# Kernel optimization log

Measured on AMD Instinct MI355X. Metric: run time of the kernel, lower is better.

## Reference

```python
import jax, jax.numpy as jnp
import numpy as np

B, D_IN, D_EXP, D_TOW, N_EXP, N_TASK = 16384, 1024, 1024, 512, 8, 4


def setup_inputs() -> dict:
    key = jax.random.key(0)
    ks = jax.random.split(key, 8)
    s_in = 1.0 / np.sqrt(D_IN)
    s_exp = 1.0 / np.sqrt(D_EXP)
    s_tow = 1.0 / np.sqrt(D_TOW)
    return {
        "x": jax.random.normal(ks[0], (B, D_IN), jnp.float32),
        # gate: ParameterList of num_experts vectors of size input_size -> [D_IN, N_EXP] matrix
        "gate_w": jax.random.normal(ks[1], (D_IN, N_EXP), jnp.float32) * s_in,
        # per-expert SLP: Linear(input_size, expert_size) + ReLU
        "exp_w": jax.random.normal(ks[2], (N_EXP, D_IN, D_EXP), jnp.float32) * s_in,
        "exp_b": jax.random.normal(ks[3], (N_EXP, D_EXP), jnp.float32) * 0.01,
        # per-task tower MLP: Linear(expert_size, tower_size) + ReLU + Linear(tower_size, 1)
        "tw1": jax.random.normal(ks[4], (N_TASK, D_EXP, D_TOW), jnp.float32) * s_exp,
        "tb1": jax.random.normal(ks[5], (N_TASK, D_TOW), jnp.float32) * 0.01,
        "tw2": jax.random.normal(ks[6], (N_TASK, D_TOW, 1), jnp.float32) * s_tow,
        "tb2": jax.random.normal(ks[7], (N_TASK, 1), jnp.float32) * 0.01,
    }


def reference(x, gate_w, exp_w, exp_b, tw1, tb1, tw2, tb2):
    # gates = x @ gate (no softmax in original)        [B, E]
    gates = x @ gate_w
    # all experts in one batched GEMM                  [E, B, D_exp]
    h = jax.nn.relu(jnp.einsum("bi,eid->ebd", x, exp_w) + exp_b[:, None, :])
    # fused gate-weighted combine (replaces the nested Python loops)
    shared = jnp.einsum("be,ebd->bd", gates, h)        # [B, D_exp]
    # per-task towers, batched over tasks
    t = jax.nn.relu(jnp.einsum("bd,tdh->tbh", shared, tw1) + tb1[:, None, :])
    outs = jnp.einsum("tbh,tho->tbo", t, tw2) + tb2[:, None, :]  # [T, B, 1]
    return outs
```

## Files before the change

### kernel.cpp

```cpp
#include <hip/hip_runtime.h>
#include <hip/hip_bf16.h>

#define B_DIM   16384
#define D_IN    1024
#define D_EXP   1024
#define D_TOW   512
#define N_EXPT  8
#define N_TASK  4

typedef _Float16 f16x8 __attribute__((ext_vector_type(8)));
typedef _Float16 f16x4 __attribute__((ext_vector_type(4)));
typedef float    f32x4 __attribute__((ext_vector_type(4)));

__device__ __forceinline__ void gll16(const void* g, void* l) {
  __builtin_amdgcn_global_load_lds(
      (const __attribute__((address_space(1))) unsigned int*)g,
      (__attribute__((address_space(3))) unsigned int*)l,
      16, 0, 0);
}

__device__ __forceinline__ f16x8 ldfrag(const _Float16* sM, int rowbase, int ks, int lane) {
  int rl = rowbase + (lane & 15);
  int ch = ((ks << 2) + (lane >> 4)) ^ (rl & 7);
  return *(const f16x8*)&sM[rl * 64 + ch * 8];
}

__global__ __launch_bounds__(256) void prep_x_kernel(
    const float* __restrict__ x, const float* __restrict__ gw,
    _Float16* __restrict__ xh, float* __restrict__ gates)
{
  __shared__ float sred[4][8];
  const int t = threadIdx.x;
  const long row = blockIdx.x;
  float4 v = ((const float4*)(x + row * D_IN))[t];
  f16x4 h;
  h[0] = (_Float16)v.x; h[1] = (_Float16)v.y; h[2] = (_Float16)v.z; h[3] = (_Float16)v.w;
  ((f16x4*)(xh + row * D_IN))[t] = h;

  float g[8];
#pragma unroll
  for (int e = 0; e < 8; ++e) g[e] = 0.f;
  const float* wp = gw + (size_t)t * 4 * 8;
  float xs[4] = {v.x, v.y, v.z, v.w};
#pragma unroll
  for (int j = 0; j < 4; ++j)
#pragma unroll
    for (int e = 0; e < 8; ++e) g[e] += xs[j] * wp[j * 8 + e];

#pragma unroll
  for (int e = 0; e < 8; ++e) {
    g[e] += __shfl_xor(g[e], 1);  g[e] += __shfl_xor(g[e], 2);
    g[e] += __shfl_xor(g[e], 4);  g[e] += __shfl_xor(g[e], 8);
    g[e] += __shfl_xor(g[e], 16); g[e] += __shfl_xor(g[e], 32);
  }
  if ((t & 63) == 0) {
#pragma unroll
    for (int e = 0; e < 8; ++e) sred[t >> 6][e] = g[e];
  }
  __syncthreads();
  if (t < 8) gates[row * 8 + t] = sred[0][t] + sred[1][t] + sred[2][t] + sred[3][t];
}

__global__ __launch_bounds__(256) void transpose_cvt_kernel(
    const float* __restrict__ in, _Float16* __restrict__ outp, int K, int N)
{
  __shared__ float tile[64][65];
  const int t = threadIdx.x;
  const int tx = t & 63, ty = t >> 6;
  const int n0 = blockIdx.x * 64;
  const int k0 = blockIdx.y * 64;
  const long s = blockIdx.z;
  const float* ip = in + s * (long)K * N;
  _Float16* op = outp + s * (long)K * N;
#pragma unroll
  for (int i = 0; i < 16; ++i) {
    int r = ty * 16 + i;
    tile[r][tx] = ip[(long)(k0 + r) * N + n0 + tx];
  }
  __syncthreads();
#pragma unroll
  for (int i = 0; i < 16; ++i) {
    int r = ty * 16 + i;
    op[(long)(n0 + r) * K + k0 + tx] = (_Float16)tile[tx][r];
  }
}

__global__ void init_out_kernel(float* __restrict__ out, const float* __restrict__ tb2) {
  int i = blockIdx.x * 256 + threadIdx.x;
  if (i < N_TASK * B_DIM) out[i] = tb2[i >> 14];
}

#define PH(SLOT, Q, STAGES, WAITS)                                             \
  do {                                                                         \
    const _Float16* sAq = &sT[SLOT][wm * 8192];                                \
    const _Float16* sBq = &sT[SLOT][16384 + (wn >> 1) * 8192];                 \
    f16x8 af[2][2];                                                            \
    _Pragma("unroll") for (int m2 = 0; m2 < 2; ++m2)                           \
      _Pragma("unroll") for (int ks = 0; ks < 2; ++ks)                         \
        af[m2][ks] = ldfrag(sAq, ((Q) * 2 + m2) * 16, ks, lane);               \
    if ((Q) == 0) {                                                            \
      _Pragma("unroll") for (int nf = 0; nf < 4; ++nf)                         \
        _Pragma("unroll") for (int ks = 0; ks < 2; ++ks)                       \
          bf[nf][ks] = ldfrag(sBq, (wn & 1) * 64 + nf * 16, ks, lane);         \
    }                                                                          \
    STAGES;                                                                    \
    asm volatile("" ::: "memory");                                             \
    if ((Q) == 0) { asm volatile("s_waitcnt lgkmcnt(8)" ::: "memory"); }       \
    __builtin_amdgcn_s_barrier();                                              \
    asm volatile("s_waitcnt lgkmcnt(0)" ::: "memory");                         \
    __builtin_amdgcn_sched_barrier(0);                                         \
    __builtin_amdgcn_s_setprio(1);                                             \
    _Pragma("unroll") for (int m2 = 0; m2 < 2; ++m2)                           \
      _Pragma("unroll") for (int nf = 0; nf < 4; ++nf)                         \
        _Pragma("unroll") for (int ks = 0; ks < 2; ++ks)                       \
          acc[(Q) * 2 + m2][nf] = __builtin_amdgcn_mfma_f32_16x16x32_f16(      \
              af[m2][ks], bf[nf][ks], acc[(Q) * 2 + m2][nf], 0, 0, 0);         \
    __builtin_amdgcn_s_setprio(0);                                             \
    WAITS;                                                                     \
    asm volatile("" ::: "memory");                                             \
    __builtin_amdgcn_s_barrier();                                              \
  } while (0)

__global__ __launch_bounds__(512, 2) void moe_expert_kernel(
    const _Float16* __restrict__ xh,
    const _Float16* __restrict__ ewT,
    const float* __restrict__ expb,
    const float* __restrict__ gates,
    _Float16* __restrict__ shout)
{
  __shared__ alignas(16) _Float16 sT[2][32768];
  __shared__ float sG[256 * 8];
  __shared__ float sBias[8 * 256];
  const int t = threadIdx.x;
  const int lane = t & 63;
  const int wave = t >> 6;
  const int wm = wave >> 2, wn = wave & 3;
  const long row0 = (long)blockIdx.x * 256;
  const int col0 = blockIdx.y * 256;

  for (int i = t; i < 256 * 8; i += 512) sG[i] = gates[row0 * 8 + i];
  for (int i = t; i < 8 * 256; i += 512)
    sBias[i] = expb[(i >> 8) * D_EXP + col0 + (i & 255)];

  const int so_t = (((t & 7) ^ ((t >> 3) & 7)) << 4);
  const char* aBase = (const char*)xh + row0 * 2048 + (size_t)(t >> 3) * 2048 + so_t;
  const char* bRoot = (const char*)ewT + (size_t)col0 * 2048 + (size_t)(t >> 3) * 2048 + so_t;
  char* sTB = (char*)&sT[0][0];

  auto SA = [&](int s, int h, int kt) {
    const char* g = aBase + (size_t)h * 262144 + (size_t)(kt & 15) * 128;
    char* d = sTB + s * 65536 + h * 16384 + t * 16;
    gll16(g, d); gll16(g + 131072, d + 8192);
    asm volatile("" ::: "memory");
  };
  auto SB = [&](int s, int h, int kt) {
    const char* g = bRoot + (size_t)(kt >> 4) * 2097152 + (size_t)h * 262144
                    + (size_t)(kt & 15) * 128;
    char* d = sTB + s * 65536 + 32768 + h * 16384 + t * 16;
    gll16(g, d); gll16(g + 131072, d + 8192);
    asm volatile("" ::: "memory");
  };

  __syncthreads();

  SB(0, 0, 0); SB(0, 1, 0);
  SA(0, 0, 0); SA(0, 1, 0);
  SB(1, 0, 1); SB(1, 1, 1);
  asm volatile("s_waitcnt vmcnt(4)" ::: "memory");
  __builtin_amdgcn_s_barrier();

  f32x4 acc[8][4] = {};
  f16x4 shacc[8][4] = {};
  f16x8 bf[4][2];

  for (int it = 0; it < 64; ++it) {
    const int kt0 = 2 * it, kt1 = 2 * it + 1;
    const bool pf = (it < 63);

    PH(0, 0, { SA(1, 0, kt1); }, {});
    PH(0, 1, { SA(1, 1, kt1); }, {});
    PH(0, 2, { if (pf) SB(0, 0, kt0 + 2); }, {});
    PH(0, 3, { if (pf) SB(0, 1, kt0 + 2); },
       { if (pf) { asm volatile("s_waitcnt vmcnt(4)" ::: "memory"); }
         else    { asm volatile("s_waitcnt vmcnt(0)" ::: "memory"); } });
    PH(1, 0, { if (pf) SA(0, 0, kt0 + 2); }, {});
    PH(1, 1, { if (pf) SA(0, 1, kt0 + 2); }, {});
    PH(1, 2, { if (pf) SB(1, 0, kt1 + 2); }, {});
    PH(1, 3, { if (pf) SB(1, 1, kt1 + 2); },
       { if (pf) { asm volatile("s_waitcnt vmcnt(4)" ::: "memory"); } });

    if ((it & 7) == 7) {
      const int e = it >> 3;
      float bias4[4];
#pragma unroll
      for (int nf = 0; nf < 4; ++nf)
        bias4[nf] = sBias[e * 256 + wn * 64 + nf * 16 + (lane & 15)];
#pragma unroll
      for (int mf = 0; mf < 8; ++mf) {
        int rbase = wm * 128 + mf * 16 + ((lane >> 4) << 2);
        float gv[4];
#pragma unroll
        for (int r = 0; r < 4; ++r) gv[r] = sG[(rbase + r) * 8 + e];
#pragma unroll
        for (int nf = 0; nf < 4; ++nf) {
          f16x4 sh = shacc[mf][nf];
#pragma unroll
          for (int r = 0; r < 4; ++r) {
            float hv = acc[mf][nf][r] + bias4[nf];
            hv = hv > 0.f ? hv : 0.f;
            sh[r] += (_Float16)(gv[r] * hv);
          }
          shacc[mf][nf] = sh;
          acc[mf][nf] = f32x4{0.f, 0.f, 0.f, 0.f};
        }
      }
    }
  }

#pragma unroll
  for (int mf = 0; mf < 8; ++mf)
#pragma unroll
    for (int r = 0; r < 4; ++r) {
      long row = row0 + wm * 128 + mf * 16 + ((lane >> 4) << 2) + r;
      _Float16* op = shout + row * D_EXP + col0 + wn * 64 + (lane & 15);
#pragma unroll
      for (int nf = 0; nf < 4; ++nf) op[nf * 16] = shacc[mf][nf][r];
    }
}

__global__ __launch_bounds__(512, 2) void moe_tower_kernel(
    const _Float16* __restrict__ sh,
    const _Float16* __restrict__ t1T,
    const float* __restrict__ tb1,
    const float* __restrict__ tw2,
    float* __restrict__ out)
{
  __shared__ alignas(16) _Float16 sT[2][32768];
  const int t = threadIdx.x;
  const int lane = t & 63;
  const int wave = t >> 6;
  const int wm = wave >> 2, wn = wave & 3;
  const long row0 = (long)blockIdx.x * 256;
  const int task = blockIdx.y >> 1;
  const int col0 = (blockIdx.y & 1) * 256;

  float b1[4], w2[4];
#pragma unroll
  for (int nf = 0; nf < 4; ++nf) {
    int col = col0 + wn * 64 + nf * 16 + (lane & 15);
    b1[nf] = tb1[task * D_TOW + col];
    w2[nf] = tw2[task * D_TOW + col];
  }
  asm volatile("s_waitcnt vmcnt(0)" ::: "memory");

  const int so_t = (((t & 7) ^ ((t >> 3) & 7)) << 4);
  const char* aBase = (const char*)sh + row0 * 2048 + (size_t)(t >> 3) * 2048 + so_t;
  const char* bRoot = (const char*)t1T + (size_t)task * (D_TOW * D_EXP * 2)
                      + (size_t)col0 * 2048 + (size_t)(t >> 3) * 2048 + so_t;
  char* sTB = (char*)&sT[0][0];

  auto SA = [&](int s, int h, int kt) {
    const char* g = aBase + (size_t)h * 262144 + (size_t)kt * 128;
    char* d = sTB + s * 65536 + h * 16384 + t * 16;
    gll16(g, d); gll16(g + 131072, d + 8192);
    asm volatile("" ::: "memory");
  };
  auto SB = [&](int s, int h, int kt) {
    const char* g = bRoot + (size_t)h * 262144 + (size_t)kt * 128;
    char* d = sTB + s * 65536 + 32768 + h * 16384 + t * 16;
    gll16(g, d); gll16(g + 131072, d + 8192);
    asm volatile("" ::: "memory");
  };

  __syncthreads();

  SB(0, 0, 0); SB(0, 1, 0);
  SA(0, 0, 0); SA(0, 1, 0);
  SB(1, 0, 1); SB(1, 1, 1);
  asm volatile("s_waitcnt vmcnt(4)" ::: "memory");
  __builtin_amdgcn_s_barrier();

  f32x4 acc[8][4] = {};
  f16x8 bf[4][2];

  for (int it = 0; it < 8; ++it) {
    const int kt0 = 2 * it, kt1 = 2 * it + 1;
    const bool pf = (it < 7);

    PH(0, 0, { SA(1, 0, kt1); }, {});
    PH(0, 1, { SA(1, 1, kt1); }, {});
    PH(0, 2, { if (pf) SB(0, 0, kt0 + 2); }, {});
    PH(0, 3, { if (pf) SB(0, 1, kt0 + 2); },
       { if (pf) { asm volatile("s_waitcnt vmcnt(4)" ::: "memory"); }
         else    { asm volatile("s_waitcnt vmcnt(0)" ::: "memory"); } });
    PH(1, 0, { if (pf) SA(0, 0, kt0 + 2); }, {});
    PH(1, 1, { if (pf) SA(0, 1, kt0 + 2); }, {});
    PH(1, 2, { if (pf) SB(1, 0, kt1 + 2); }, {});
    PH(1, 3, { if (pf) SB(1, 1, kt1 + 2); },
       { if (pf) { asm volatile("s_waitcnt vmcnt(4)" ::: "memory"); } });
  }

#pragma unroll
  for (int mf = 0; mf < 8; ++mf)
#pragma unroll
    for (int r = 0; r < 4; ++r) {
      float ssum = 0.f;
#pragma unroll
      for (int nf = 0; nf < 4; ++nf) {
        float v = acc[mf][nf][r] + b1[nf];
        v = v > 0.f ? v : 0.f;
        ssum += v * w2[nf];
      }
      ssum += __shfl_xor(ssum, 1);
      ssum += __shfl_xor(ssum, 2);
      ssum += __shfl_xor(ssum, 4);
      ssum += __shfl_xor(ssum, 8);
      if ((lane & 15) == 0) {
        long row = row0 + wm * 128 + mf * 16 + ((lane >> 4) << 2) + r;
        atomicAdd(&out[(size_t)task * B_DIM + row], ssum);
      }
    }
}

extern "C" void kernel_launch(void* const* d_in, const int* in_sizes, int n_in,
                              void* d_out, int out_size, void* d_ws, size_t ws_size,
                              hipStream_t stream) {
  const float* x    = (const float*)d_in[0];
  const float* gw   = (const float*)d_in[1];
  const float* expw = (const float*)d_in[2];
  const float* expb = (const float*)d_in[3];
  const float* tw1  = (const float*)d_in[4];
  const float* tb1  = (const float*)d_in[5];
  const float* tw2  = (const float*)d_in[6];
  const float* tb2  = (const float*)d_in[7];
  float* out = (float*)d_out;

  char* ws = (char*)d_ws;
  _Float16* xh  = (_Float16*)ws;  ws += (size_t)B_DIM * D_IN * 2;
  _Float16* ewT = (_Float16*)ws;  ws += (size_t)N_EXPT * D_IN * D_EXP * 2;
  _Float16* t1T = (_Float16*)ws;  ws += (size_t)N_TASK * D_TOW * D_EXP * 2;
  _Float16* shh = (_Float16*)ws;  ws += (size_t)B_DIM * D_EXP * 2;
  float* gates  = (float*)ws;     ws += (size_t)B_DIM * N_EXPT * 4;

  prep_x_kernel<<<B_DIM, 256, 0, stream>>>(x, gw, xh, gates);
  transpose_cvt_kernel<<<dim3(D_EXP / 64, D_IN / 64, N_EXPT), 256, 0, stream>>>(
      expw, ewT, D_IN, D_EXP);
  transpose_cvt_kernel<<<dim3(D_TOW / 64, D_EXP / 64, N_TASK), 256, 0, stream>>>(
      tw1, t1T, D_EXP, D_TOW);
  init_out_kernel<<<(N_TASK * B_DIM + 255) / 256, 256, 0, stream>>>(out, tb2);
  moe_expert_kernel<<<dim3(B_DIM / 256, D_EXP / 256), 512, 0, stream>>>(
      xh, ewT, expb, gates, shh);
  moe_tower_kernel<<<dim3(B_DIM / 256, N_TASK * (D_TOW / 256)), 512, 0, stream>>>(
      shh, t1T, tb1, tw2, out);
}
```

Baseline: 448.8 us.

## Simplify GEMM pipeline to per-k-tile double buffering and remap block order

Replaces the fine-grained four-phase interleaved schedule, which staged loads between MFMA quarters with setprio and per-phase barriers, with a simpler loop. Each k-tile now does a full compute, one barrier, a prefetch two tiles ahead into the freed buffer, and a wait plus barrier. Both GEMM kernels switch to a 1D grid with a swizzled block-to-tile mapping so that co-resident blocks share A or B tiles in L2. Expert bias is stored as fp16 in LDS. The trade-off is fewer barriers but less overlap of memory loads with MFMA inside a tile, plus a slight precision change in the bias.

```diff
diff --git a/kernel.cpp b/kernel.cpp
--- a/kernel.cpp
+++ b/kernel.cpp
@@ -90,36 +90,28 @@
   if (i < N_TASK * B_DIM) out[i] = tb2[i >> 14];
 }
 
-#define PH(SLOT, Q, STAGES, WAITS)                                             \
+#define KTILE_COMPUTE(CUR)                                                     \
   do {                                                                         \
-    const _Float16* sAq = &sT[SLOT][wm * 8192];                                \
-    const _Float16* sBq = &sT[SLOT][16384 + (wn >> 1) * 8192];                 \
-    f16x8 af[2][2];                                                            \
-    _Pragma("unroll") for (int m2 = 0; m2 < 2; ++m2)                           \
+    const _Float16* sA = &sT[CUR][wm * 8192];                                  \
+    const _Float16* sB = &sT[CUR][16384 + (wn >> 1) * 8192];                   \
+    f16x8 bf[4][2];                                                            \
+    _Pragma("unroll") for (int nf = 0; nf < 4; ++nf)                           \
       _Pragma("unroll") for (int ks = 0; ks < 2; ++ks)                         \
-        af[m2][ks] = ldfrag(sAq, ((Q) * 2 + m2) * 16, ks, lane);               \
-    if ((Q) == 0) {                                                            \
-      _Pragma("unroll") for (int nf = 0; nf < 4; ++nf)                         \
+        bf[nf][ks] = ldfrag(sB, (wn & 1) * 64 + nf * 16, ks, lane);            \
+    _Pragma("unroll") for (int Q = 0; Q < 4; ++Q) {                            \
+      f16x8 af[2][2];                                                          \
+      _Pragma("unroll") for (int m2 = 0; m2 < 2; ++m2)                         \
         _Pragma("unroll") for (int ks = 0; ks < 2; ++ks)                       \
-          bf[nf][ks] = ldfrag(sBq, (wn & 1) * 64 + nf * 16, ks, lane);         \
+          af[m2][ks] = ldfrag(sA, (Q * 2 + m2) * 16, ks, lane);                \
+      _Pragma("unroll") for (int m2 = 0; m2 < 2; ++m2)                         \
+        _Pragma("unroll") for (int nf = 0; nf < 4; ++nf)                       \
+          _Pragma("unroll") for (int ks = 0; ks < 2; ++ks)                     \
+            acc[Q * 2 + m2][nf] = __builtin_amdgcn_mfma_f32_16x16x32_f16(      \
+                af[m2][ks], bf[nf][ks], acc[Q * 2 + m2][nf], 0, 0, 0);         \
     }                                                                          \
-    STAGES;                                                                    \
-    asm volatile("" ::: "memory");                                             \
-    if ((Q) == 0) { asm volatile("s_waitcnt lgkmcnt(8)" ::: "memory"); }       \
-    __builtin_amdgcn_s_barrier();                                              \
-    asm volatile("s_waitcnt lgkmcnt(0)" ::: "memory");                         \
-    __builtin_amdgcn_sched_barrier(0);                                         \
-    __builtin_amdgcn_s_setprio(1);                                             \
-    _Pragma("unroll") for (int m2 = 0; m2 < 2; ++m2)                           \
-      _Pragma("unroll") for (int nf = 0; nf < 4; ++nf)                         \
-        _Pragma("unroll") for (int ks = 0; ks < 2; ++ks)                       \
-          acc[(Q) * 2 + m2][nf] = __builtin_amdgcn_mfma_f32_16x16x32_f16(      \
-              af[m2][ks], bf[nf][ks], acc[(Q) * 2 + m2][nf], 0, 0, 0);         \
-    __builtin_amdgcn_s_setprio(0);                                             \
-    WAITS;                                                                     \
-    asm volatile("" ::: "memory");                                             \
-    __builtin_amdgcn_s_barrier();                                              \
   } while (0)
+
+#define FENCE asm volatile("" ::: "memory")
 
 __global__ __launch_bounds__(512, 2) void moe_expert_kernel(
     const _Float16* __restrict__ xh,
@@ -130,71 +122,72 @@
 {
   __shared__ alignas(16) _Float16 sT[2][32768];
   __shared__ float sG[256 * 8];
-  __shared__ float sBias[8 * 256];
+  __shared__ _Float16 sBiasH[8 * 256];
   const int t = threadIdx.x;
   const int lane = t & 63;
   const int wave = t >> 6;
   const int wm = wave >> 2, wn = wave & 3;
-  const long row0 = (long)blockIdx.x * 256;
-  const int col0 = blockIdx.y * 256;
+
+  const int h = blockIdx.x;
+  const int bx = 2 * (h >> 3) + (h & 1);
+  const int by = (h & 7) >> 1;
+  const long row0 = (long)bx * 256;
+  const int col0 = by * 256;
 
   for (int i = t; i < 256 * 8; i += 512) sG[i] = gates[row0 * 8 + i];
   for (int i = t; i < 8 * 256; i += 512)
-    sBias[i] = expb[(i >> 8) * D_EXP + col0 + (i & 255)];
+    sBiasH[i] = (_Float16)expb[(i >> 8) * D_EXP + col0 + (i & 255)];
 
   const int so_t = (((t & 7) ^ ((t >> 3) & 7)) << 4);
   const char* aBase = (const char*)xh + row0 * 2048 + (size_t)(t >> 3) * 2048 + so_t;
   const char* bRoot = (const char*)ewT + (size_t)col0 * 2048 + (size_t)(t >> 3) * 2048 + so_t;
   char* sTB = (char*)&sT[0][0];
 
-  auto SA = [&](int s, int h, int kt) {
-    const char* g = aBase + (size_t)h * 262144 + (size_t)(kt & 15) * 128;
-    char* d = sTB + s * 65536 + h * 16384 + t * 16;
+  auto SA = [&](int s, int hh, int kt) {
+    const char* g = aBase + (size_t)hh * 262144 + (size_t)(kt & 15) * 128;
+    char* d = sTB + s * 65536 + hh * 16384 + t * 16;
     gll16(g, d); gll16(g + 131072, d + 8192);
-    asm volatile("" ::: "memory");
+    FENCE;
   };
-  auto SB = [&](int s, int h, int kt) {
-    const char* g = bRoot + (size_t)(kt >> 4) * 2097152 + (size_t)h * 262144
+  auto SB = [&](int s, int hh, int kt) {
+    const char* g = bRoot + (size_t)(kt >> 4) * 2097152 + (size_t)hh * 262144
                     + (size_t)(kt & 15) * 128;
-    char* d = sTB + s * 65536 + 32768 + h * 16384 + t * 16;
+    char* d = sTB + s * 65536 + 32768 + hh * 16384 + t * 16;
     gll16(g, d); gll16(g + 131072, d + 8192);
-    asm volatile("" ::: "memory");
+    FENCE;
   };
 
   __syncthreads();
 
-  SB(0, 0, 0); SB(0, 1, 0);
-  SA(0, 0, 0); SA(0, 1, 0);
-  SB(1, 0, 1); SB(1, 1, 1);
-  asm volatile("s_waitcnt vmcnt(4)" ::: "memory");
+  SA(0, 0, 0); SA(0, 1, 0); SB(0, 0, 0); SB(0, 1, 0);
+  SA(1, 0, 1); SA(1, 1, 1); SB(1, 0, 1); SB(1, 1, 1);
+  asm volatile("s_waitcnt vmcnt(8)" ::: "memory");
   __builtin_amdgcn_s_barrier();
+  FENCE;
 
   f32x4 acc[8][4] = {};
   f16x4 shacc[8][4] = {};
-  f16x8 bf[4][2];
-
-  for (int it = 0; it < 64; ++it) {
-    const int kt0 = 2 * it, kt1 = 2 * it + 1;
-    const bool pf = (it < 63);
-
-    PH(0, 0, { SA(1, 0, kt1); }, {});
-    PH(0, 1, { SA(1, 1, kt1); }, {});
-    PH(0, 2, { if (pf) SB(0, 0, kt0 + 2); }, {});
-    PH(0, 3, { if (pf) SB(0, 1, kt0 + 2); },
-       { if (pf) { asm volatile("s_waitcnt vmcnt(4)" ::: "memory"); }
-         else    { asm volatile("s_waitcnt vmcnt(0)" ::: "memory"); } });
-    PH(1, 0, { if (pf) SA(0, 0, kt0 + 2); }, {});
-    PH(1, 1, { if (pf) SA(0, 1, kt0 + 2); }, {});
-    PH(1, 2, { if (pf) SB(1, 0, kt1 + 2); }, {});
-    PH(1, 3, { if (pf) SB(1, 1, kt1 + 2); },
-       { if (pf) { asm volatile("s_waitcnt vmcnt(4)" ::: "memory"); } });
-
-    if ((it & 7) == 7) {
-      const int e = it >> 3;
+
+  for (int kt = 0; kt < 128; ++kt) {
+    const int cur = kt & 1;
+
+    KTILE_COMPUTE(cur);
+
+    FENCE;
+    __builtin_amdgcn_s_barrier();
+    FENCE;
+
+    if (kt < 126) {
+      SA(cur, 0, kt + 2); SA(cur, 1, kt + 2);
+      SB(cur, 0, kt + 2); SB(cur, 1, kt + 2);
+    }
+
+    if ((kt & 15) == 15) {
+      const int e = kt >> 4;
       float bias4[4];
 #pragma unroll
       for (int nf = 0; nf < 4; ++nf)
-        bias4[nf] = sBias[e * 256 + wn * 64 + nf * 16 + (lane & 15)];
+        bias4[nf] = (float)sBiasH[e * 256 + wn * 64 + nf * 16 + (lane & 15)];
 #pragma unroll
       for (int mf = 0; mf < 8; ++mf) {
         int rbase = wm * 128 + mf * 16 + ((lane >> 4) << 2);
@@ -214,6 +207,13 @@
           acc[mf][nf] = f32x4{0.f, 0.f, 0.f, 0.f};
         }
       }
+    }
+
+    if (kt < 127) {
+      if (kt < 126) { asm volatile("s_waitcnt vmcnt(8)" ::: "memory"); }
+      else          { asm volatile("s_waitcnt vmcnt(0)" ::: "memory"); }
+      __builtin_amdgcn_s_barrier();
+      FENCE;
     }
   }
 
@@ -240,9 +240,13 @@
   const int lane = t & 63;
   const int wave = t >> 6;
   const int wm = wave >> 2, wn = wave & 3;
-  const long row0 = (long)blockIdx.x * 256;
-  const int task = blockIdx.y >> 1;
-  const int col0 = (blockIdx.y & 1) * 256;
+
+  const int h = blockIdx.x;
+  const int by = h & 7;
+  const int bx = h >> 3;
+  const long row0 = (long)bx * 256;
+  const int task = by >> 1;
+  const int col0 = (by & 1) * 256;
 
   float b1[4], w2[4];
 #pragma unroll
@@ -259,45 +263,49 @@
                       + (size_t)col0 * 2048 + (size_t)(t >> 3) * 2048 + so_t;
   char* sTB = (char*)&sT[0][0];
 
-  auto SA = [&](int s, int h, int kt) {
-    const char* g = aBase + (size_t)h * 262144 + (size_t)kt * 128;
-    char* d = sTB + s * 65536 + h * 16384 + t * 16;
+  auto SA = [&](int s, int hh, int kt) {
+    const char* g = aBase + (size_t)hh * 262144 + (size_t)kt * 128;
+    char* d = sTB + s * 65536 + hh * 16384 + t * 16;
     gll16(g, d); gll16(g + 131072, d + 8192);
-    asm volatile("" ::: "memory");
+    FENCE;
   };
-  auto SB = [&](int s, int h, int kt) {
-    const char* g = bRoot + (size_t)h * 262144 + (size_t)kt * 128;
-    char* d = sTB + s * 65536 + 32768 + h * 16384 + t * 16;
+  auto SB = [&](int s, int hh, int kt) {
+    const char* g = bRoot + (size_t)hh * 262144 + (size_t)kt * 128;
+    char* d = sTB + s * 65536 + 32768 + hh * 16384 + t * 16;
     gll16(g, d); gll16(g + 131072, d + 8192);
-    asm volatile("" ::: "memory");
+    FENCE;
   };
 
   __syncthreads();
 
-  SB(0, 0, 0); SB(0, 1, 0);
-  SA(0, 0, 0); SA(0, 1, 0);
-  SB(1, 0, 1); SB(1, 1, 1);
-  asm volatile("s_waitcnt vmcnt(4)" ::: "memory");
+  SA(0, 0, 0); SA(0, 1, 0); SB(0, 0, 0); SB(0, 1, 0);
+  SA(1, 0, 1); SA(1, 1, 1); SB(1, 0, 1); SB(1, 1, 1);
+  asm volatile("s_waitcnt vmcnt(8)" ::: "memory");
   __builtin_amdgcn_s_barrier();
+  FENCE;
 
   f32x4 acc[8][4] = {};
-  f16x8 bf[4][2];
-
-  for (int it = 0; it < 8; ++it) {
-    const int kt0 = 2 * it, kt1 = 2 * it + 1;
-    const bool pf = (it < 7);
-
-    PH(0, 0, { SA(1, 0, kt1); }, {});
-    PH(0, 1, { SA(1, 1, kt1); }, {});
-    PH(0, 2, { if (pf) SB(0, 0, kt0 + 2); }, {});
-    PH(0, 3, { if (pf) SB(0, 1, kt0 + 2); },
-       { if (pf) { asm volatile("s_waitcnt vmcnt(4)" ::: "memory"); }
-         else    { asm volatile("s_waitcnt vmcnt(0)" ::: "memory"); } });
-    PH(1, 0, { if (pf) SA(0, 0, kt0 + 2); }, {});
-    PH(1, 1, { if (pf) SA(0, 1, kt0 + 2); }, {});
-    PH(1, 2, { if (pf) SB(1, 0, kt1 + 2); }, {});
-    PH(1, 3, { if (pf) SB(1, 1, kt1 + 2); },
-       { if (pf) { asm volatile("s_waitcnt vmcnt(4)" ::: "memory"); } });
+
+  for (int kt = 0; kt < 16; ++kt) {
+    const int cur = kt & 1;
+
+    KTILE_COMPUTE(cur);
+
+    FENCE;
+    __builtin_amdgcn_s_barrier();
+    FENCE;
+
+    if (kt < 14) {
+      SA(cur, 0, kt + 2); SA(cur, 1, kt + 2);
+      SB(cur, 0, kt + 2); SB(cur, 1, kt + 2);
+    }
+
+    if (kt < 15) {
+      if (kt < 14) { asm volatile("s_waitcnt vmcnt(8)" ::: "memory"); }
+      else         { asm volatile("s_waitcnt vmcnt(0)" ::: "memory"); }
+      __builtin_amdgcn_s_barrier();
+      FENCE;
+    }
   }
 
 #pragma unroll
@@ -348,8 +356,6 @@
   transpose_cvt_kernel<<<dim3(D_TOW / 64, D_EXP / 64, N_TASK), 256, 0, stream>>>(
       tw1, t1T, D_EXP, D_TOW);
   init_out_kernel<<<(N_TASK * B_DIM + 255) / 256, 256, 0, stream>>>(out, tb2);
-  moe_expert_kernel<<<dim3(B_DIM / 256, D_EXP / 256), 512, 0, stream>>>(
-      xh, ewT, expb, gates, shh);
-  moe_tower_kernel<<<dim3(B_DIM / 256, N_TASK * (D_TOW / 256)), 512, 0, stream>>>(
-      shh, t1T, tb1, tw2, out);
-}
+  moe_expert_kernel<<<256, 512, 0, stream>>>(xh, ewT, expb, gates, shh);
+  moe_tower_kernel<<<512, 512, 0, stream>>>(shh, t1T, tb1, tw2, out);
+}
```

New measurement: 416.1 us. 1.08x faster.
